# Performance work log

Measured on AMD Instinct MI355X. Metric: run time of the kernel, lower is better.

Reference implementation:

```python
import jax, jax.numpy as jnp
import numpy as np

V, NLAB, NLAYERS, DI, DM, DS, DD, K = 32000, 9, 2, 768, 1536, 16, 96, 4
B, S = 2, 2048
EPS = 1e-6


def setup_inputs() -> dict:
    key = jax.random.key(0)
    ks = jax.random.split(key, 12)
    n = lambda k, shape, s=0.02: jax.random.normal(k, shape, jnp.float32) * s
    return {
        "input_ids": jax.random.randint(ks[0], (B, S), 0, V, dtype=jnp.int32),
        "attention_mask": jnp.ones((B, S), jnp.int32),
        "emb": n(ks[1], (V, DI)),
        "norm_w": jnp.ones((NLAYERS, DI), jnp.float32),
        "in_proj_w": n(ks[2], (NLAYERS, 2 * DM, DI)),
        "conv_w": n(ks[3], (NLAYERS, DM, K), 0.1),
        "conv_b": jnp.zeros((NLAYERS, DM), jnp.float32),
        "sB_w": n(ks[4], (NLAYERS, DS, DM)),
        "sC_w": n(ks[5], (NLAYERS, DS, DM)),
        "sD1_w": n(ks[6], (NLAYERS, DD, DM)),
        "sD2_w": n(ks[7], (NLAYERS, DM, DD)),
        "A": jnp.tile(jnp.arange(1, DS + 1, dtype=jnp.float32), (NLAYERS, DM, 1)),
        "Dp": jnp.ones((NLAYERS, DM), jnp.float32),
        "out_w": n(ks[8], (NLAYERS, DI, DM)),
        "cls_w": n(ks[9], (NLAB, DI)),
        "cls_b": jnp.zeros((NLAB,), jnp.float32),
    }


def _rmsnorm(x, w):
    return x * jax.lax.rsqrt(jnp.mean(x * x, axis=-1, keepdims=True) + EPS) * w


def _mamba_block(x, norm_w, Wi, cw, cb, WB, WC, W1, W2, A, Dp, Wo):
    # x: (b, l, d_input)
    h = _rmsnorm(x, norm_w)
    a, gate = jnp.split(h @ Wi.T, 2, axis=-1)  # each (b, l, DM)
    # causal depthwise conv1d, kernel K, left-pad K-1 (== Conv1d(pad=K-1)[..., :l])
    L = a.shape[1]
    ap = jnp.pad(a, ((0, 0), (K - 1, 0), (0, 0)))
    conv = cb + sum(ap[:, i:i + L, :] * cw[:, i] for i in range(K))
    a = jax.nn.silu(conv)
    # selective SSM
    Bm = a @ WB.T                                   # (b, l, DS)
    Cm = a @ WC.T                                   # (b, l, DS)
    delta = jax.nn.softplus(Dp + (a @ W1.T) @ W2.T)  # (b, l, DM)
    A_bar = jnp.exp(delta[..., None] * (-A))         # (b, l, DM, DS)
    X_bar = (delta * a)[..., None] * Bm[:, :, None, :]  # (b, l, DM, DS)

    def comb(c1, c2):
        a1, x1 = c1
        a2, x2 = c2
        return a1 * a2, a2 * x1 + x2

    _, hid = jax.lax.associative_scan(comb, (A_bar, X_bar), axis=1)
    y = jnp.einsum('blds,bls->bld', hid, Cm) + Dp * a
    y = y * jax.nn.silu(gate)
    return y @ Wo.T


def _forward(input_ids, attention_mask, emb, norm_w, in_proj_w, conv_w, conv_b,
             sB_w, sC_w, sD1_w, sD2_w, A, Dp, out_w, cls_w, cls_b):
    x = emb[input_ids] * attention_mask[..., None].astype(emb.dtype)
    for i in range(NLAYERS):  # residual Mamba layers
        x = _mamba_block(x, norm_w[i], in_proj_w[i], conv_w[i], conv_b[i],
                         sB_w[i], sC_w[i], sD1_w[i], sD2_w[i], A[i], Dp[i], out_w[i]) + x
    # dropout is identity at inference
    return x @ cls_w.T + cls_b  # logits (b, l, num_labels)


def reference(input_ids, attention_mask, emb, norm_w, in_proj_w, conv_w, conv_b,
              sB_w, sC_w, sD1_w, sD2_w, A, Dp, out_w, cls_w, cls_b):
    return _forward(input_ids, attention_mask, emb, norm_w, in_proj_w, conv_w, conv_b,
                    sB_w, sC_w, sD1_w, sD2_w, A, Dp, out_w, cls_w, cls_b)
```

## Files before the change

kernel.cpp:

```cpp
#include <hip/hip_runtime.h>
#include <hip/hip_bf16.h>
#include <math.h>

#define NLAB 9
#define NL   2
#define DI   768
#define DM   1536
#define DS   16
#define KC   4
#define DD   96
#define BB   2
#define SS   2048
#define TT   (BB*SS)
#define EPSF 1e-6f

#define NCH  32
#define CL   (SS/NCH)

#define NW   128
#define KS   8
#define KSL  (DM/KS)

typedef __attribute__((ext_vector_type(4))) float f32x4;
typedef __attribute__((ext_vector_type(8))) short bf16x8;
typedef __attribute__((ext_vector_type(4))) unsigned short us4;

__device__ __forceinline__ float siluf(float x) { return x / (1.f + __expf(-x)); }
__device__ __forceinline__ float softplusf(float x) { return x > 15.f ? x : log1pf(__expf(x)); }

__device__ __forceinline__ unsigned short f2bf(float f) {
    unsigned u = __float_as_uint(f);
    return (unsigned short)((u + 0x7fffu + ((u >> 16) & 1u)) >> 16);
}

__global__ void f32_to_bf16(const float* __restrict__ src,
                            unsigned short* __restrict__ dst, int n)
{
    int i = (blockIdx.x * 256 + threadIdx.x) * 8;
    if (i >= n) return;
    float4 a = *(const float4*)(src + i);
    float4 b = *(const float4*)(src + i + 4);
    union { unsigned short s[8]; uint4 v; } o;
    o.s[0] = f2bf(a.x); o.s[1] = f2bf(a.y); o.s[2] = f2bf(a.z); o.s[3] = f2bf(a.w);
    o.s[4] = f2bf(b.x); o.s[5] = f2bf(b.y); o.s[6] = f2bf(b.z); o.s[7] = f2bf(b.w);
    *(uint4*)(dst + i) = o.v;
}

__global__ void embed_kernel(const int* __restrict__ ids, const int* __restrict__ mask,
                             const float* __restrict__ emb, float* __restrict__ x)
{
    int t = blockIdx.x;
    int i = threadIdx.x;
    float m = (float)mask[t];
    int id = ids[t];
    float4 v = ((const float4*)(emb + (size_t)id * DI))[i];
    v.x *= m; v.y *= m; v.z *= m; v.w *= m;
    ((float4*)(x + (size_t)t * DI))[i] = v;
}

__global__ void rmsnorm_kernel(const float* __restrict__ x, const float* __restrict__ w,
                               unsigned short* __restrict__ h)
{
    __shared__ float red[4];
    int t = blockIdx.x;
    const float* xr = x + (size_t)t * DI;
    float ss = 0.f;
    for (int i = threadIdx.x; i < DI; i += 256) { float v = xr[i]; ss += v * v; }
    #pragma unroll
    for (int m = 1; m < 64; m <<= 1) ss += __shfl_xor(ss, m, 64);
    if ((threadIdx.x & 63) == 0) red[threadIdx.x >> 6] = ss;
    __syncthreads();
    float scale = rsqrtf((red[0] + red[1] + red[2] + red[3]) * (1.f / DI) + EPSF);
    for (int i = threadIdx.x; i < DI; i += 256)
        h[(size_t)t * DI + i] = f2bf(xr[i] * scale * w[i]);
}

__global__ __launch_bounds__(256) void gemm_bf16(
    const unsigned short* __restrict__ A, const unsigned short* __restrict__ B,
    const float* __restrict__ Rres, const float* __restrict__ bias,
    float* __restrict__ C, int M, int N, int K,
    int lda, int ldb, int ldc, int act)
{
    __shared__ unsigned short As[128 * 32];
    __shared__ unsigned short Bs[128 * 32];
    const int tid = threadIdx.x;
    const int wave = tid >> 6, lane = tid & 63;
    const int bm = blockIdx.y * 128, bn = blockIdx.x * 128;
    const int wm = (wave >> 1) * 64, wn = (wave & 1) * 64;
    const int lr = lane & 15, kh = lane >> 4;

    f32x4 acc[4][4] = {};

    const unsigned short* Arow = A + (size_t)bm * lda;
    const unsigned short* Brow = B + (size_t)bn * ldb;

    for (int kt = 0; kt < K; kt += 32) {
        #pragma unroll
        for (int it = 0; it < 2; ++it) {
            int rbase = it * 64 + wave * 16;
            int row = rbase + (lane >> 2);
            int c8 = (lane & 3) * 8;
            __builtin_amdgcn_global_load_lds(
                (const __attribute__((address_space(1))) unsigned int*)(Arow + (size_t)row * lda + kt + c8),
                (__attribute__((address_space(3))) unsigned int*)(As + rbase * 32),
                16, 0, 0);
            __builtin_amdgcn_global_load_lds(
                (const __attribute__((address_space(1))) unsigned int*)(Brow + (size_t)row * ldb + kt + c8),
                (__attribute__((address_space(3))) unsigned int*)(Bs + rbase * 32),
                16, 0, 0);
        }
        __syncthreads();

        bf16x8 af[4], bfr[4];
        #pragma unroll
        for (int i = 0; i < 4; ++i)
            af[i] = *(const bf16x8*)&As[(wm + i * 16 + lr) * 32 + kh * 8];
        #pragma unroll
        for (int j = 0; j < 4; ++j)
            bfr[j] = *(const bf16x8*)&Bs[(wn + j * 16 + lr) * 32 + kh * 8];
        #pragma unroll
        for (int i = 0; i < 4; ++i)
            #pragma unroll
            for (int j = 0; j < 4; ++j)
                acc[i][j] = __builtin_amdgcn_mfma_f32_16x16x32_bf16(af[i], bfr[j], acc[i][j], 0, 0, 0);
        __syncthreads();
    }

    #pragma unroll
    for (int i = 0; i < 4; ++i) {
        #pragma unroll
        for (int j = 0; j < 4; ++j) {
            #pragma unroll
            for (int r = 0; r < 4; ++r) {
                int row = bm + wm + i * 16 + kh * 4 + r;
                int col = bn + wn + j * 16 + lr;
                float v = acc[i][j][r];
                if (bias) v += bias[col];
                if (act == 1) v = softplusf(v);
                if (Rres) v += Rres[(size_t)row * ldc + col];
                C[(size_t)row * ldc + col] = v;
            }
        }
    }
}

__global__ __launch_bounds__(256) void gemm_skinny_bf16(
    const unsigned short* __restrict__ A, const unsigned short* __restrict__ B,
    float* __restrict__ Part)
{
    __shared__ unsigned short As[128 * 32];
    __shared__ unsigned short Bs[128 * 32];
    const int tid = threadIdx.x;
    const int wave = tid >> 6, lane = tid & 63;
    const int bm = blockIdx.x * 128;
    const int ks = blockIdx.y;
    const int k0 = ks * KSL;
    const int wm = (wave >> 1) * 64, wn = (wave & 1) * 64;
    const int lr = lane & 15, kh = lane >> 4;

    f32x4 acc[4][4] = {};

    const unsigned short* Arow = A + (size_t)bm * DM;
    const unsigned short* Brow = B;

    for (int kt = 0; kt < KSL; kt += 32) {
        #pragma unroll
        for (int it = 0; it < 2; ++it) {
            int rbase = it * 64 + wave * 16;
            int row = rbase + (lane >> 2);
            int c8 = (lane & 3) * 8;
            __builtin_amdgcn_global_load_lds(
                (const __attribute__((address_space(1))) unsigned int*)(Arow + (size_t)row * DM + k0 + kt + c8),
                (__attribute__((address_space(3))) unsigned int*)(As + rbase * 32),
                16, 0, 0);
            __builtin_amdgcn_global_load_lds(
                (const __attribute__((address_space(1))) unsigned int*)(Brow + (size_t)row * DM + k0 + kt + c8),
                (__attribute__((address_space(3))) unsigned int*)(Bs + rbase * 32),
                16, 0, 0);
        }
        __syncthreads();

        bf16x8 af[4], bfr[4];
        #pragma unroll
        for (int i = 0; i < 4; ++i)
            af[i] = *(const bf16x8*)&As[(wm + i * 16 + lr) * 32 + kh * 8];
        #pragma unroll
        for (int j = 0; j < 4; ++j)
            bfr[j] = *(const bf16x8*)&Bs[(wn + j * 16 + lr) * 32 + kh * 8];
        #pragma unroll
        for (int i = 0; i < 4; ++i)
            #pragma unroll
            for (int j = 0; j < 4; ++j)
                acc[i][j] = __builtin_amdgcn_mfma_f32_16x16x32_bf16(af[i], bfr[j], acc[i][j], 0, 0, 0);
        __syncthreads();
    }

    float* out = Part + (size_t)ks * TT * NW;
    #pragma unroll
    for (int i = 0; i < 4; ++i) {
        #pragma unroll
        for (int j = 0; j < 4; ++j) {
            #pragma unroll
            for (int r = 0; r < 4; ++r) {
                int row = bm + wm + i * 16 + kh * 4 + r;
                int col = wn + j * 16 + lr;
                out[(size_t)row * NW + col] = acc[i][j][r];
            }
        }
    }
}

__global__ void skinny_reduce(const float* __restrict__ Part,
                              float* __restrict__ BCD, unsigned short* __restrict__ dd16)
{
    int idx = blockIdx.x * 256 + threadIdx.x;
    float s = 0.f;
    #pragma unroll
    for (int ks = 0; ks < KS; ++ks)
        s += Part[(size_t)ks * TT * NW + idx];
    BCD[idx] = s;
    int col = idx & (NW - 1);
    if (col >= 32)
        dd16[(size_t)(idx >> 7) * DD + (col - 32)] = f2bf(s);
}

__global__ void conv_silu_kernel(const float* __restrict__ proj, const float* __restrict__ cw,
                                 const float* __restrict__ cb, float* __restrict__ aconv,
                                 unsigned short* __restrict__ aconv16)
{
    int t = blockIdx.x;
    int d = blockIdx.y * 256 + threadIdx.x;
    int p = t & (SS - 1);
    float acc = cb[d];
    #pragma unroll
    for (int j = 0; j < KC; ++j) {
        int pp = p - (KC - 1) + j;
        if (pp >= 0)
            acc += cw[d * KC + j] * proj[(size_t)(t - (KC - 1) + j) * (2 * DM) + d];
    }
    float v = siluf(acc);
    aconv[(size_t)t * DM + d] = v;
    aconv16[(size_t)t * DM + d] = f2bf(v);
}

__global__ void concat_w_kernel(const float* __restrict__ WB, const float* __restrict__ WC,
                                const float* __restrict__ W1, unsigned short* __restrict__ Wcat16)
{
    int l = blockIdx.y;
    int row = blockIdx.x;
    const float* src;
    if (row < 16)      src = WB + (size_t)l * DS * DM + (size_t)row * DM;
    else if (row < 32) src = WC + (size_t)l * DS * DM + (size_t)(row - 16) * DM;
    else               src = W1 + (size_t)l * DD * DM + (size_t)(row - 32) * DM;
    unsigned short* dst = Wcat16 + ((size_t)l * NW + row) * DM;
    for (int i = threadIdx.x; i < DM / 4; i += 256) {
        float4 v = ((const float4*)src)[i];
        us4 u = { f2bf(v.x), f2bf(v.y), f2bf(v.z), f2bf(v.w) };
        *(us4*)(dst + i * 4) = u;
    }
}

__global__ __launch_bounds__(256) void scan_pass1(
    const float* __restrict__ delta, const float* __restrict__ aconv,
    const float* __restrict__ BCD, const float* __restrict__ Amat,
    float2* __restrict__ PQ)
{
    __shared__ float4 sB4[CL][DS / 4];
    int b = blockIdx.z, c = blockIdx.y;
    int d = blockIdx.x * 256 + threadIdx.x;
    size_t rowbase = (size_t)b * SS + (size_t)c * CL;

    for (int i = threadIdx.x; i < CL * DS; i += 256)
        ((float*)sB4)[i] = BCD[(rowbase + (i >> 4)) * NW + (i & 15)];
    __syncthreads();

    float negA[DS], hid[DS];
    #pragma unroll
    for (int s = 0; s < DS; ++s) {
        negA[s] = -Amat[(size_t)d * DS + s];
        hid[s] = 0.f;
    }
    float cum = 0.f;

    const float* dp = delta + rowbase * DM + d;
    const float* ap = aconv + rowbase * DM + d;
    for (int t = 0; t < CL; ++t) {
        float dt = dp[(size_t)t * DM];
        float av = ap[(size_t)t * DM];
        cum += dt;
        float xv = dt * av;
        #pragma unroll
        for (int j = 0; j < DS / 4; ++j) {
            float4 bv = sB4[t][j];
            hid[4*j+0] = __expf(dt * negA[4*j+0]) * hid[4*j+0] + xv * bv.x;
            hid[4*j+1] = __expf(dt * negA[4*j+1]) * hid[4*j+1] + xv * bv.y;
            hid[4*j+2] = __expf(dt * negA[4*j+2]) * hid[4*j+2] + xv * bv.z;
            hid[4*j+3] = __expf(dt * negA[4*j+3]) * hid[4*j+3] + xv * bv.w;
        }
    }
    float2* out = PQ + ((size_t)(b * NCH + c) * DM + d) * DS;
    #pragma unroll
    for (int s = 0; s < DS; ++s)
        out[s] = make_float2(__expf(cum * negA[s]), hid[s]);
}

__global__ void scan_carry(float2* __restrict__ PQ)
{
    int idx = blockIdx.x * 256 + threadIdx.x;
    int b = idx / (DM * DS);
    int r = idx - b * (DM * DS);
    float carry = 0.f;
    for (int c = 0; c < NCH; ++c) {
        size_t o = (size_t)(b * NCH + c) * (DM * DS) + r;
        float2 pq = PQ[o];
        PQ[o].x = carry;
        carry = pq.x * carry + pq.y;
    }
}

__global__ __launch_bounds__(256) void scan_pass2(
    const float* __restrict__ delta, const float* __restrict__ aconv,
    const float* __restrict__ BCD,
    const float* __restrict__ proj, const float* __restrict__ Amat,
    const float* __restrict__ Dp, const float2* __restrict__ PQ,
    unsigned short* __restrict__ y)
{
    __shared__ float4 sB4[CL][DS / 4];
    __shared__ float4 sC4[CL][DS / 4];
    int b = blockIdx.z, c = blockIdx.y;
    int d = blockIdx.x * 256 + threadIdx.x;
    size_t rowbase = (size_t)b * SS + (size_t)c * CL;

    for (int i = threadIdx.x; i < CL * DS; i += 256) {
        size_t row = rowbase + (i >> 4);
        ((float*)sB4)[i] = BCD[row * NW + (i & 15)];
        ((float*)sC4)[i] = BCD[row * NW + 16 + (i & 15)];
    }
    __syncthreads();

    float negA[DS], hid[DS];
    const float2* pin = PQ + ((size_t)(b * NCH + c) * DM + d) * DS;
    #pragma unroll
    for (int s = 0; s < DS; ++s) {
        negA[s] = -Amat[(size_t)d * DS + s];
        hid[s] = pin[s].x;
    }
    float Dpd = Dp[d];

    const float* dp = delta + rowbase * DM + d;
    const float* ap = aconv + rowbase * DM + d;
    const float* gp = proj + rowbase * (2 * DM) + DM + d;
    unsigned short* yp = y + rowbase * DM + d;

    for (int t = 0; t < CL; ++t) {
        float dt = dp[(size_t)t * DM];
        float av = ap[(size_t)t * DM];
        float g  = gp[(size_t)t * (2 * DM)];
        float xv = dt * av;
        float acc0 = 0.f, acc1 = 0.f, acc2 = 0.f, acc3 = 0.f;
        #pragma unroll
        for (int j = 0; j < DS / 4; ++j) {
            float4 bv = sB4[t][j];
            float4 cv = sC4[t][j];
            hid[4*j+0] = __expf(dt * negA[4*j+0]) * hid[4*j+0] + xv * bv.x;
            hid[4*j+1] = __expf(dt * negA[4*j+1]) * hid[4*j+1] + xv * bv.y;
            hid[4*j+2] = __expf(dt * negA[4*j+2]) * hid[4*j+2] + xv * bv.z;
            hid[4*j+3] = __expf(dt * negA[4*j+3]) * hid[4*j+3] + xv * bv.w;
            acc0 += hid[4*j+0] * cv.x;
            acc1 += hid[4*j+1] * cv.y;
            acc2 += hid[4*j+2] * cv.z;
            acc3 += hid[4*j+3] * cv.w;
        }
        float contrib = (acc0 + acc1) + (acc2 + acc3);
        yp[(size_t)t * DM] = f2bf((contrib + Dpd * av) * siluf(g));
    }
}

__global__ void cls_kernel(const float* __restrict__ x, const float* __restrict__ W,
                           const float* __restrict__ bias, float* __restrict__ out)
{
    int t = blockIdx.x;
    int lane = threadIdx.x;
    const float* xr = x + (size_t)t * DI;
    float acc[NLAB];
    #pragma unroll
    for (int n = 0; n < NLAB; ++n) acc[n] = 0.f;
    for (int i = lane; i < DI; i += 64) {
        float xv = xr[i];
        #pragma unroll
        for (int n = 0; n < NLAB; ++n) acc[n] += xv * W[(size_t)n * DI + i];
    }
    #pragma unroll
    for (int n = 0; n < NLAB; ++n)
        #pragma unroll
        for (int m = 1; m < 64; m <<= 1) acc[n] += __shfl_xor(acc[n], m, 64);
    if (lane < NLAB) out[(size_t)t * NLAB + lane] = acc[lane] + bias[lane];
}

extern "C" void kernel_launch(void* const* d_in, const int* in_sizes, int n_in,
                              void* d_out, int out_size, void* d_ws, size_t ws_size,
                              hipStream_t stream)
{
    const int*   ids    = (const int*)d_in[0];
    const int*   mask   = (const int*)d_in[1];
    const float* emb    = (const float*)d_in[2];
    const float* norm_w = (const float*)d_in[3];
    const float* Wi     = (const float*)d_in[4];
    const float* conv_w = (const float*)d_in[5];
    const float* conv_b = (const float*)d_in[6];
    const float* sB_w   = (const float*)d_in[7];
    const float* sC_w   = (const float*)d_in[8];
    const float* sD1_w  = (const float*)d_in[9];
    const float* sD2_w  = (const float*)d_in[10];
    const float* Amat   = (const float*)d_in[11];
    const float* Dp     = (const float*)d_in[12];
    const float* out_w  = (const float*)d_in[13];
    const float* cls_w  = (const float*)d_in[14];
    const float* cls_b  = (const float*)d_in[15];
    float* logits = (float*)d_out;

    float* ws = (float*)d_ws;
    size_t off = 0;
    float* x     = ws + off; off += (size_t)TT * DI;
    float* proj  = ws + off; off += (size_t)TT * 2 * DM;
    float* aconv = ws + off; off += (size_t)TT * DM;
    float* delta = ws + off; off += (size_t)TT * DM;
    float* BCD   = ws + off; off += (size_t)TT * NW;
    float* Part  = ws + off; off += (size_t)KS * TT * NW;
    float2* PQ   = (float2*)(ws + off); off += (size_t)BB * NCH * DM * DS * 2;
    unsigned short* y16   = (unsigned short*)(ws + off); off += (size_t)TT * DM / 2;
    unsigned short* aconv16 = (unsigned short*)(ws + off); off += (size_t)TT * DM / 2;
    unsigned short* Wi16  = (unsigned short*)(ws + off); off += (size_t)NL * 2 * DM * DI / 2;
    unsigned short* Wo16  = (unsigned short*)(ws + off); off += (size_t)NL * DI * DM / 2;
    unsigned short* W216  = (unsigned short*)(ws + off); off += (size_t)NL * DM * DD / 2;
    unsigned short* dd16  = (unsigned short*)(ws + off); off += (size_t)TT * DD / 2;
    unsigned short* Wcat16 = (unsigned short*)(ws + off); off += (size_t)NL * NW * DM / 2;
    if (ws_size < off * sizeof(float)) return;

    unsigned short* h16 = (unsigned short*)delta;

    embed_kernel<<<TT, DI / 4, 0, stream>>>(ids, mask, emb, x);
    concat_w_kernel<<<dim3(NW, NL), 256, 0, stream>>>(sB_w, sC_w, sD1_w, Wcat16);

    f32_to_bf16<<<(NL * 2 * DM * DI / 8 + 255) / 256, 256, 0, stream>>>(Wi, Wi16, NL * 2 * DM * DI);
    f32_to_bf16<<<(NL * DI * DM / 8 + 255) / 256, 256, 0, stream>>>(out_w, Wo16, NL * DI * DM);
    f32_to_bf16<<<(NL * DM * DD / 8 + 255) / 256, 256, 0, stream>>>(sD2_w, W216, NL * DM * DD);

    for (int l = 0; l < NL; ++l) {
        const float* cw_l  = conv_w + (size_t)l * DM * KC;
        const float* cb_l  = conv_b + (size_t)l * DM;
        const float* A_l   = Amat  + (size_t)l * DM * DS;
        const float* Dp_l  = Dp    + (size_t)l * DM;
        const float* nw_l  = norm_w + (size_t)l * DI;
        const unsigned short* Wi16_l  = Wi16  + (size_t)l * 2 * DM * DI;
        const unsigned short* Wo16_l  = Wo16  + (size_t)l * DI * DM;
        const unsigned short* W216_l  = W216  + (size_t)l * DM * DD;
        const unsigned short* Wcat16_l = Wcat16 + (size_t)l * NW * DM;

        rmsnorm_kernel<<<TT, 256, 0, stream>>>(x, nw_l, h16);

        gemm_bf16<<<dim3(2 * DM / 128, TT / 128), 256, 0, stream>>>(
            h16, Wi16_l, nullptr, nullptr, proj, TT, 2 * DM, DI, DI, DI, 2 * DM, 0);

        conv_silu_kernel<<<dim3(TT, DM / 256), 256, 0, stream>>>(proj, cw_l, cb_l, aconv, aconv16);

        gemm_skinny_bf16<<<dim3(TT / 128, KS), 256, 0, stream>>>(aconv16, Wcat16_l, Part);
        skinny_reduce<<<TT * NW / 256, 256, 0, stream>>>(Part, BCD, dd16);

        gemm_bf16<<<dim3(DM / 128, TT / 128), 256, 0, stream>>>(
            dd16, W216_l, nullptr, Dp_l, delta, TT, DM, DD, DD, DD, DM, 1);

        scan_pass1<<<dim3(DM / 256, NCH, BB), 256, 0, stream>>>(
            delta, aconv, BCD, A_l, PQ);
        scan_carry<<<BB * DM * DS / 256, 256, 0, stream>>>(PQ);
        scan_pass2<<<dim3(DM / 256, NCH, BB), 256, 0, stream>>>(
            delta, aconv, BCD, proj, A_l, Dp_l, PQ, y16);

        gemm_bf16<<<dim3(DI / 128, TT / 128), 256, 0, stream>>>(
            y16, Wo16_l, x, nullptr, x, TT, DI, DM, DM, DM, DI, 0);
    }

    cls_kernel<<<TT, 64, 0, stream>>>(x, cls_w, cls_b, logits);
}
```

Baseline: 771.1 us.

## Interleave delta and conv output, double scan chunks, alias Part with PQ

Delta and the conv/SiLU activation are stored interleaved as float2, so each scan step issues one 8-byte load instead of two separate strided loads. To do this, the GEMM epilogue gains an output stride parameter. The scan chunk count is doubled so the scan passes launch more blocks and each has a shorter serial loop, at the cost of a larger carry buffer and a bigger carry pass. The skinny-GEMM partial buffer and the scan carry buffer now share workspace memory. The strided GEMM writes to the interleaved buffer are less coalesced.

After: 742.1 us. 1.04x faster.

```diff
diff --git a/kernel.cpp b/kernel.cpp
--- a/kernel.cpp
+++ b/kernel.cpp
@@ -14,7 +14,7 @@
 #define TT   (BB*SS)
 #define EPSF 1e-6f
 
-#define NCH  32
+#define NCH  64
 #define CL   (SS/NCH)
 
 #define NW   128
@@ -79,7 +79,7 @@
     const unsigned short* __restrict__ A, const unsigned short* __restrict__ B,
     const float* __restrict__ Rres, const float* __restrict__ bias,
     float* __restrict__ C, int M, int N, int K,
-    int lda, int ldb, int ldc, int act)
+    int lda, int ldb, int ldc, int act, int cstride)
 {
     __shared__ unsigned short As[128 * 32];
     __shared__ unsigned short Bs[128 * 32];
@@ -138,7 +138,7 @@
                 if (bias) v += bias[col];
                 if (act == 1) v = softplusf(v);
                 if (Rres) v += Rres[(size_t)row * ldc + col];
-                C[(size_t)row * ldc + col] = v;
+                C[((size_t)row * ldc + col) * cstride] = v;
             }
         }
     }
@@ -225,7 +225,7 @@
 }
 
 __global__ void conv_silu_kernel(const float* __restrict__ proj, const float* __restrict__ cw,
-                                 const float* __restrict__ cb, float* __restrict__ aconv,
+                                 const float* __restrict__ cb, float2* __restrict__ dav,
                                  unsigned short* __restrict__ aconv16)
 {
     int t = blockIdx.x;
@@ -239,7 +239,7 @@
             acc += cw[d * KC + j] * proj[(size_t)(t - (KC - 1) + j) * (2 * DM) + d];
     }
     float v = siluf(acc);
-    aconv[(size_t)t * DM + d] = v;
+    dav[(size_t)t * DM + d].y = v;
     aconv16[(size_t)t * DM + d] = f2bf(v);
 }
 
@@ -261,7 +261,7 @@
 }
 
 __global__ __launch_bounds__(256) void scan_pass1(
-    const float* __restrict__ delta, const float* __restrict__ aconv,
+    const float2* __restrict__ dav,
     const float* __restrict__ BCD, const float* __restrict__ Amat,
     float2* __restrict__ PQ)
 {
@@ -282,11 +282,10 @@
     }
     float cum = 0.f;
 
-    const float* dp = delta + rowbase * DM + d;
-    const float* ap = aconv + rowbase * DM + d;
+    const float2* pv = dav + rowbase * DM + d;
     for (int t = 0; t < CL; ++t) {
-        float dt = dp[(size_t)t * DM];
-        float av = ap[(size_t)t * DM];
+        float2 da = pv[(size_t)t * DM];
+        float dt = da.x, av = da.y;
         cum += dt;
         float xv = dt * av;
         #pragma unroll
@@ -319,7 +318,7 @@
 }
 
 __global__ __launch_bounds__(256) void scan_pass2(
-    const float* __restrict__ delta, const float* __restrict__ aconv,
+    const float2* __restrict__ dav,
     const float* __restrict__ BCD,
     const float* __restrict__ proj, const float* __restrict__ Amat,
     const float* __restrict__ Dp, const float2* __restrict__ PQ,
@@ -347,14 +346,13 @@
     }
     float Dpd = Dp[d];
 
-    const float* dp = delta + rowbase * DM + d;
-    const float* ap = aconv + rowbase * DM + d;
+    const float2* pv = dav + rowbase * DM + d;
     const float* gp = proj + rowbase * (2 * DM) + DM + d;
     unsigned short* yp = y + rowbase * DM + d;
 
     for (int t = 0; t < CL; ++t) {
-        float dt = dp[(size_t)t * DM];
-        float av = ap[(size_t)t * DM];
+        float2 da = pv[(size_t)t * DM];
+        float dt = da.x, av = da.y;
         float g  = gp[(size_t)t * (2 * DM)];
         float xv = dt * av;
         float acc0 = 0.f, acc1 = 0.f, acc2 = 0.f, acc3 = 0.f;
@@ -423,21 +421,23 @@
     size_t off = 0;
     float* x     = ws + off; off += (size_t)TT * DI;
     float* proj  = ws + off; off += (size_t)TT * 2 * DM;
-    float* aconv = ws + off; off += (size_t)TT * DM;
-    float* delta = ws + off; off += (size_t)TT * DM;
+    float2* dav  = (float2*)(ws + off); off += (size_t)TT * DM * 2;
     float* BCD   = ws + off; off += (size_t)TT * NW;
-    float* Part  = ws + off; off += (size_t)KS * TT * NW;
-    float2* PQ   = (float2*)(ws + off); off += (size_t)BB * NCH * DM * DS * 2;
-    unsigned short* y16   = (unsigned short*)(ws + off); off += (size_t)TT * DM / 2;
+    size_t scratch_sz = (size_t)BB * NCH * DM * DS * 2;
+    size_t part_sz = (size_t)KS * TT * NW;
+    if (part_sz > scratch_sz) scratch_sz = part_sz;
+    float* Part  = ws + off;
+    float2* PQ   = (float2*)(ws + off); off += scratch_sz;
+    unsigned short* y16     = (unsigned short*)(ws + off); off += (size_t)TT * DM / 2;
     unsigned short* aconv16 = (unsigned short*)(ws + off); off += (size_t)TT * DM / 2;
-    unsigned short* Wi16  = (unsigned short*)(ws + off); off += (size_t)NL * 2 * DM * DI / 2;
-    unsigned short* Wo16  = (unsigned short*)(ws + off); off += (size_t)NL * DI * DM / 2;
-    unsigned short* W216  = (unsigned short*)(ws + off); off += (size_t)NL * DM * DD / 2;
-    unsigned short* dd16  = (unsigned short*)(ws + off); off += (size_t)TT * DD / 2;
-    unsigned short* Wcat16 = (unsigned short*)(ws + off); off += (size_t)NL * NW * DM / 2;
+    unsigned short* Wi16    = (unsigned short*)(ws + off); off += (size_t)NL * 2 * DM * DI / 2;
+    unsigned short* Wo16    = (unsigned short*)(ws + off); off += (size_t)NL * DI * DM / 2;
+    unsigned short* W216    = (unsigned short*)(ws + off); off += (size_t)NL * DM * DD / 2;
+    unsigned short* dd16    = (unsigned short*)(ws + off); off += (size_t)TT * DD / 2;
+    unsigned short* Wcat16  = (unsigned short*)(ws + off); off += (size_t)NL * NW * DM / 2;
     if (ws_size < off * sizeof(float)) return;
 
-    unsigned short* h16 = (unsigned short*)delta;
+    unsigned short* h16 = (unsigned short*)dav;
 
     embed_kernel<<<TT, DI / 4, 0, stream>>>(ids, mask, emb, x);
     concat_w_kernel<<<dim3(NW, NL), 256, 0, stream>>>(sB_w, sC_w, sD1_w, Wcat16);
@@ -460,24 +460,23 @@
         rmsnorm_kernel<<<TT, 256, 0, stream>>>(x, nw_l, h16);
 
         gemm_bf16<<<dim3(2 * DM / 128, TT / 128), 256, 0, stream>>>(
-            h16, Wi16_l, nullptr, nullptr, proj, TT, 2 * DM, DI, DI, DI, 2 * DM, 0);
-
-        conv_silu_kernel<<<dim3(TT, DM / 256), 256, 0, stream>>>(proj, cw_l, cb_l, aconv, aconv16);
+            h16, Wi16_l, nullptr, nullptr, proj, TT, 2 * DM, DI, DI, DI, 2 * DM, 0, 1);
+
+        conv_silu_kernel<<<dim3(TT, DM / 256), 256, 0, stream>>>(proj, cw_l, cb_l, dav, aconv16);
 
         gemm_skinny_bf16<<<dim3(TT / 128, KS), 256, 0, stream>>>(aconv16, Wcat16_l, Part);
         skinny_reduce<<<TT * NW / 256, 256, 0, stream>>>(Part, BCD, dd16);
 
         gemm_bf16<<<dim3(DM / 128, TT / 128), 256, 0, stream>>>(
-            dd16, W216_l, nullptr, Dp_l, delta, TT, DM, DD, DD, DD, DM, 1);
-
-        scan_pass1<<<dim3(DM / 256, NCH, BB), 256, 0, stream>>>(
-            delta, aconv, BCD, A_l, PQ);
+            dd16, W216_l, nullptr, Dp_l, (float*)dav, TT, DM, DD, DD, DD, DM, 1, 2);
+
+        scan_pass1<<<dim3(DM / 256, NCH, BB), 256, 0, stream>>>(dav, BCD, A_l, PQ);
         scan_carry<<<BB * DM * DS / 256, 256, 0, stream>>>(PQ);
         scan_pass2<<<dim3(DM / 256, NCH, BB), 256, 0, stream>>>(
-            delta, aconv, BCD, proj, A_l, Dp_l, PQ, y16);
+            dav, BCD, proj, A_l, Dp_l, PQ, y16);
 
         gemm_bf16<<<dim3(DI / 128, TT / 128), 256, 0, stream>>>(
-            y16, Wo16_l, x, nullptr, x, TT, DI, DM, DM, DM, DI, 0);
+            y16, Wo16_l, x, nullptr, x, TT, DI, DM, DM, DM, DI, 0, 1);
     }
 
     cls_kernel<<<TT, 64, 0, stream>>>(x, cls_w, cls_b, logits);
```
